# Optimization experiments

Hardware: AMD Instinct MI355X
Metric: run time of the kernel (lower is better)

Reference implementation:

```python
import jax, jax.numpy as jnp
import numpy as np

E = 512      # embed_dim
H = 8        # num_heads
D = E // H   # head_dim = 64
R = 32       # rot_dims (partial rotary)
THETA = 10000.0


def _rope(x):
    # x: [B, H, S, D]; rotate first R dims (interleaved pairs, lucidrains-style)
    S = x.shape[-2]
    inv_freq = THETA ** (-jnp.arange(0, R, 2, dtype=jnp.float32) / R)  # [R/2]
    ang = jnp.arange(S, dtype=jnp.float32)[:, None] * inv_freq          # [S, R/2]
    c, s = jnp.cos(ang), jnp.sin(ang)
    xr, xp = x[..., :R], x[..., R:]
    x1, x2 = xr[..., 0::2], xr[..., 1::2]
    rot = jnp.stack([x1 * c - x2 * s, x1 * s + x2 * c], axis=-1).reshape(xr.shape)
    return jnp.concatenate([rot, xp], axis=-1)


def setup_inputs() -> dict:
    key = jax.random.key(0)
    k1, k2, k3, k4 = jax.random.split(key, 4)
    B, S = 4, 2048
    x = jax.random.normal(k1, (B, S, E), dtype=jnp.float32)
    input_mask = jax.random.randint(k2, (B, S), 0, 2).astype(bool)
    W_in = jax.random.normal(k3, (3 * E, E), dtype=jnp.float32) / np.sqrt(E).astype(np.float32)
    W_out = jax.random.normal(k4, (E, E), dtype=jnp.float32) / np.sqrt(E).astype(np.float32)
    return {"x": x, "input_mask": input_mask, "W_in": W_in, "W_out": W_out}


def reference(x, input_mask, W_in, W_out):
    B, S, _ = x.shape
    # fused QKV projection (Linear, no bias): x @ W_in.T -> [B,S,3E]
    qkv = (x @ W_in.T).reshape(B, S, 3, H, D).transpose(2, 0, 3, 1, 4)  # [3,B,H,S,D]
    q, k, v = qkv[0], qkv[1], qkv[2]
    q = _rope(q)
    k = _rope(k)
    # mask: causal AND (both tokens valid OR diagonal)
    causal = jnp.tril(jnp.ones((S, S), dtype=bool))
    inv = ~input_mask                                  # [B,S]
    cross = inv[:, None, :] | inv[:, :, None]          # [B,S,S]
    square = (~cross) | jnp.eye(S, dtype=bool)         # diagonal forced True
    full = causal[None, :, :] & square                 # [B,S,S]
    scores = jnp.einsum('bhsd,bhtd->bhst', q, k) / np.float32(np.sqrt(D))
    scores = jnp.where(full[:, None, :, :], scores, -jnp.inf)
    probs = jax.nn.softmax(scores, axis=-1)
    attn = jnp.einsum('bhst,bhtd->bhsd', probs, v)
    attn = attn.transpose(0, 2, 1, 3).reshape(B, S, E)
    return attn @ W_out.T
```

## Files before the change

kernel.cpp:

```cpp
#include <hip/hip_runtime.h>
#include <math.h>

#define B_ 4
#define S_ 2048
#define E_ 512
#define H_ 8
#define D_ 64

typedef short bf16x8 __attribute__((ext_vector_type(8)));
typedef float f32x4 __attribute__((ext_vector_type(4)));

__device__ inline short f2bf(float f) {
  union { float f; unsigned u; } v; v.f = f;
  unsigned r = v.u + 0x7FFF + ((v.u >> 16) & 1);
  return (short)(r >> 16);
}
__device__ inline short f2bf_fast(float f) {
  union { float f; unsigned u; } v; v.f = f;
  return (short)((v.u + 0x8000u) >> 16);
}
__device__ inline float bf2f(short s) {
  union { unsigned u; float f; } v; v.u = ((unsigned)(unsigned short)s) << 16;
  return v.f;
}
__device__ __forceinline__ float exp2_hw(float x) {
  float r; asm("v_exp_f32 %0, %1" : "=v"(r) : "v"(x)); return r;
}

__device__ __forceinline__ void gload16(const short* g, short* l) {
  __builtin_amdgcn_global_load_lds(
      (__attribute__((address_space(1))) void*)g,
      (__attribute__((address_space(3))) void*)l, 16, 0, 0);
}

__global__ __launch_bounds__(256) void cvt_all(
    const float* __restrict__ x, const float* __restrict__ win,
    const float* __restrict__ wout, short* __restrict__ xb,
    short* __restrict__ winb, short* __restrict__ woutb) {
  int bid = blockIdx.x;
  const float* src; short* dst; int i;
  if (bid < 4096)      { src = x;    dst = xb;    i = bid * 256 + threadIdx.x; }
  else if (bid < 4864) { src = win;  dst = winb;  i = (bid - 4096) * 256 + threadIdx.x; }
  else                 { src = wout; dst = woutb; i = (bid - 4864) * 256 + threadIdx.x; }
  float4 f = ((const float4*)src)[i];
  short4 o;
  o.x = f2bf(f.x); o.y = f2bf(f.y); o.z = f2bf(f.z); o.w = f2bf(f.w);
  ((short4*)dst)[i] = o;
}

__global__ __launch_bounds__(256, 6) void gemm_qkv_mfma(
    const short* __restrict__ Xb,
    const short* __restrict__ Wb,
    short* __restrict__ qb, short* __restrict__ kb, short* __restrict__ vbT) {
  __shared__ __align__(16) short As[2 * 128 * 32];
  __shared__ __align__(16) short Bs[2 * 64 * 32];
  const int tid = threadIdx.x;
  const int w = tid >> 6, lane = tid & 63;
  const int l15 = lane & 15, quad = lane >> 4;
  const int wm = w & 1, wn = w >> 1;
  const int m0 = blockIdx.x * 128;
  const int n0 = blockIdx.y * 64;

  const int srow = tid >> 2, sch = (tid & 3) * 8;
  const short* gA0 = Xb + (size_t)(m0 + srow) * E_ + sch;
  const short* gA1 = Xb + (size_t)(m0 + srow + 64) * E_ + sch;
  const short* gB0 = Wb + (size_t)(n0 + srow) * E_ + sch;

  f32x4 acc[4][2];
  for (int mt = 0; mt < 4; ++mt)
    for (int nt = 0; nt < 2; ++nt) acc[mt][nt] = (f32x4){0.f, 0.f, 0.f, 0.f};

  gload16(gA0, &As[tid * 8]);
  gload16(gA1, &As[2048 + tid * 8]);
  gload16(gB0, &Bs[tid * 8]);
  gA0 += 32; gA1 += 32; gB0 += 32;
  __syncthreads();

  int cur = 0;
  for (int t = 0; t < 16; ++t) {
    if (t < 15) {
      const int nbA = (cur ^ 1) * 4096, nbB = (cur ^ 1) * 2048;
      gload16(gA0, &As[nbA + tid * 8]);
      gload16(gA1, &As[nbA + 2048 + tid * 8]);
      gload16(gB0, &Bs[nbB + tid * 8]);
      gA0 += 32; gA1 += 32; gB0 += 32;
    }
    const int cbA = cur * 4096, cbB = cur * 2048;
    bf16x8 a[4], bfr[2];
#pragma unroll
    for (int mt = 0; mt < 4; ++mt)
      a[mt] = *(const bf16x8*)&As[cbA + (wm * 64 + mt * 16 + l15) * 32 + quad * 8];
#pragma unroll
    for (int nt = 0; nt < 2; ++nt)
      bfr[nt] = *(const bf16x8*)&Bs[cbB + (wn * 32 + nt * 16 + l15) * 32 + quad * 8];
#pragma unroll
    for (int mt = 0; mt < 4; ++mt)
#pragma unroll
      for (int nt = 0; nt < 2; ++nt)
        acc[mt][nt] = __builtin_amdgcn_mfma_f32_16x16x32_bf16(a[mt], bfr[nt], acc[mt][nt], 0, 0, 0);
    __syncthreads();
    cur ^= 1;
  }

  const int t3 = n0 >> 9;
  for (int nt = 0; nt < 2; ++nt) {
    const int n = n0 + wn * 32 + nt * 16 + l15;
    const int h = (n >> 6) & 7;
    const int d = n & 63;
    const bool dorope = (t3 < 2) && (d < 32);
    const float sgn = (d & 1) ? 1.f : -1.f;
    const float fr = dorope ? exp2f((float)(d >> 1) * -0.8304820237f) : 0.f;
    for (int mt = 0; mt < 4; ++mt) {
      for (int i = 0; i < 4; ++i) {
        const int m = m0 + wm * 64 + mt * 16 + quad * 4 + i;
        const int b = m >> 11, s = m & (S_ - 1);
        float val = acc[mt][nt][i];
        float pv = __shfl_xor(val, 1, 64);
        float outv = val;
        if (dorope) {
          float ang = (float)s * fr;
          float sn, cs;
          sincosf(ang, &sn, &cs);
          outv = val * cs + pv * sgn * sn;
        }
        if (t3 == 2)
          vbT[((size_t)(b * 8 + h) * D_ + d) * S_ + s] = f2bf(outv);
        else {
          short* dst = (t3 == 0) ? qb : kb;
          dst[(((size_t)(b * 8 + h)) * S_ + s) * D_ + d] = f2bf(outv);
        }
      }
    }
  }
}

__global__ __launch_bounds__(256) void gemm_out_mfma(
    const short* __restrict__ Ab, const short* __restrict__ Wb,
    float* __restrict__ out) {
  __shared__ __align__(16) short As[2 * 128 * 32];
  __shared__ __align__(16) short Bs[2 * 64 * 32];
  const int tid = threadIdx.x;
  const int w = tid >> 6, lane = tid & 63;
  const int l15 = lane & 15, quad = lane >> 4;
  const int wm = w & 1, wn = w >> 1;
  const int m0 = blockIdx.x * 128;
  const int n0 = blockIdx.y * 64;

  const int srow = tid >> 2, sch = (tid & 3) * 8;
  const short* gA0 = Ab + (size_t)(m0 + srow) * E_ + sch;
  const short* gA1 = Ab + (size_t)(m0 + srow + 64) * E_ + sch;
  const short* gB0 = Wb + (size_t)(n0 + srow) * E_ + sch;

  f32x4 acc[4][2];
  for (int mt = 0; mt < 4; ++mt)
    for (int nt = 0; nt < 2; ++nt) acc[mt][nt] = (f32x4){0.f, 0.f, 0.f, 0.f};

  gload16(gA0, &As[tid * 8]);
  gload16(gA1, &As[2048 + tid * 8]);
  gload16(gB0, &Bs[tid * 8]);
  gA0 += 32; gA1 += 32; gB0 += 32;
  __syncthreads();

  int cur = 0;
  for (int t = 0; t < 16; ++t) {
    if (t < 15) {
      const int nbA = (cur ^ 1) * 4096, nbB = (cur ^ 1) * 2048;
      gload16(gA0, &As[nbA + tid * 8]);
      gload16(gA1, &As[nbA + 2048 + tid * 8]);
      gload16(gB0, &Bs[nbB + tid * 8]);
      gA0 += 32; gA1 += 32; gB0 += 32;
    }
    const int cbA = cur * 4096, cbB = cur * 2048;
    bf16x8 a[4], bfr[2];
#pragma unroll
    for (int mt = 0; mt < 4; ++mt)
      a[mt] = *(const bf16x8*)&As[cbA + (wm * 64 + mt * 16 + l15) * 32 + quad * 8];
#pragma unroll
    for (int nt = 0; nt < 2; ++nt)
      bfr[nt] = *(const bf16x8*)&Bs[cbB + (wn * 32 + nt * 16 + l15) * 32 + quad * 8];
#pragma unroll
    for (int mt = 0; mt < 4; ++mt)
#pragma unroll
      for (int nt = 0; nt < 2; ++nt)
        acc[mt][nt] = __builtin_amdgcn_mfma_f32_16x16x32_bf16(a[mt], bfr[nt], acc[mt][nt], 0, 0, 0);
    __syncthreads();
    cur ^= 1;
  }
  for (int mt = 0; mt < 4; ++mt)
    for (int nt = 0; nt < 2; ++nt) {
      const int n = n0 + wn * 32 + nt * 16 + l15;
      for (int i = 0; i < 4; ++i) {
        const int m = m0 + wm * 64 + mt * 16 + quad * 4 + i;
        out[(size_t)m * E_ + n] = acc[mt][nt][i];
      }
    }
}

__global__ __launch_bounds__(256) void flash_mfma(
    const short* __restrict__ qb, const short* __restrict__ kb,
    const short* __restrict__ vbT, const int* __restrict__ maskp,
    short* __restrict__ pb0, short* __restrict__ pb1,
    float* __restrict__ lb0, float* __restrict__ lb1,
    short* __restrict__ ob) {
  __shared__ __align__(16) short Ks[64][72];
  __shared__ __align__(16) short VT[64][72];
  __shared__ __align__(16) short Pl[4][16][72];
  __shared__ float kbias[64];
  const int tid = threadIdx.x;
  const int w = tid >> 6, lane = tid & 63;
  const int l15 = lane & 15, quad = lane >> 4;
  const int bid = blockIdx.x;
  const int u = bid & 7, v = bid >> 3;
  const int bh = (u << 2) | (v & 3);
  const int w2 = v >> 2;
  const int pair = w2 & 15;
  const int kh = w2 >> 4;
  const int b = bh >> 3, hd = bh & 7;
  const short* qbase = qb + (size_t)bh * S_ * D_;
  const short* kbase = kb + (size_t)bh * S_ * D_;
  const short* vtb   = vbT + (size_t)bh * D_ * S_;
  short* PB = kh ? pb1 : pb0;
  float* LB = kh ? lb1 : lb0;
  const float c2 = 0.1803368801f;
  bf16x8 ones;
  for (int j = 0; j < 8; ++j) ones[j] = (short)0x3F80;

  for (int seg = 0; seg < 2; ++seg) {
    const int qt = (seg == 0) ? pair : 31 - pair;
    const int r0 = qt * 64;
    const int mid = (qt + 2) >> 1;
    const int lo = kh ? mid : 0;
    const int hi = kh ? (qt + 1) : mid;
    bf16x8 aq[2];
    {
      const short* qrow = qbase + (size_t)(r0 + 16 * w + l15) * D_;
      aq[0] = *(const bf16x8*)&qrow[quad * 8];
      aq[1] = *(const bf16x8*)&qrow[32 + quad * 8];
    }
    f32x4 o[4], lsum;
    for (int no = 0; no < 4; ++no) o[no] = (f32x4){0.f, 0.f, 0.f, 0.f};
    lsum = (f32x4){0.f, 0.f, 0.f, 0.f};

    for (int kt = lo; kt < hi; ++kt) {
      const int t0 = kt * 64;
      __syncthreads();
      for (int l = 0; l < 2; ++l) {
        int idx = tid + 256 * l;
        int row = idx >> 3, ch = (idx & 7) * 8;
        *(bf16x8*)&Ks[row][ch] = *(const bf16x8*)(kbase + (size_t)(t0 + row) * D_ + ch);
        *(bf16x8*)&VT[row][ch] = *(const bf16x8*)(vtb + (size_t)row * S_ + t0 + ch);
      }
      if (tid < 64)
        kbias[tid] = maskp[b * S_ + t0 + tid] ? -23.08312f : -1.0e38f;
      __syncthreads();
      f32x4 sfr[4];
      for (int nb = 0; nb < 4; ++nb) sfr[nb] = (f32x4){0.f, 0.f, 0.f, 0.f};
      for (int nb = 0; nb < 4; ++nb)
        for (int ks = 0; ks < 2; ++ks) {
          bf16x8 bk = *(const bf16x8*)&Ks[l15 + 16 * nb][32 * ks + quad * 8];
          sfr[nb] = __builtin_amdgcn_mfma_f32_16x16x32_bf16(aq[ks], bk, sfr[nb], 0, 0, 0);
        }
      if (kt < qt) {
        for (int nb = 0; nb < 4; ++nb) {
          const float bb = kbias[l15 + 16 * nb];
          for (int i = 0; i < 4; ++i)
            Pl[w][quad * 4 + i][l15 + 16 * nb] = f2bf_fast(exp2_hw(sfr[nb][i] * c2 + bb));
        }
      } else {
        for (int nb = 0; nb < 4; ++nb) {
          const int tg = l15 + 16 * nb;
          const float bb = kbias[l15 + 16 * nb];
          for (int i = 0; i < 4; ++i) {
            const float bbi = (tg > 16 * w + quad * 4 + i) ? -1.0e38f : bb;
            Pl[w][quad * 4 + i][l15 + 16 * nb] = f2bf_fast(exp2_hw(sfr[nb][i] * c2 + bbi));
          }
        }
      }
      asm volatile("s_waitcnt lgkmcnt(0)" ::: "memory");
      bf16x8 ap0 = *(const bf16x8*)&Pl[w][l15][quad * 8];
      bf16x8 ap1 = *(const bf16x8*)&Pl[w][l15][32 + quad * 8];
      for (int no = 0; no < 4; ++no) {
        bf16x8 bv0 = *(const bf16x8*)&VT[16 * no + l15][quad * 8];
        bf16x8 bv1 = *(const bf16x8*)&VT[16 * no + l15][32 + quad * 8];
        o[no] = __builtin_amdgcn_mfma_f32_16x16x32_bf16(ap0, bv0, o[no], 0, 0, 0);
        o[no] = __builtin_amdgcn_mfma_f32_16x16x32_bf16(ap1, bv1, o[no], 0, 0, 0);
      }
      lsum = __builtin_amdgcn_mfma_f32_16x16x32_bf16(ap0, ones, lsum, 0, 0, 0);
      lsum = __builtin_amdgcn_mfma_f32_16x16x32_bf16(ap1, ones, lsum, 0, 0, 0);
    }
    for (int i = 0; i < 4; ++i) {
      const int s = r0 + 16 * w + quad * 4 + i;
      const int qm = maskp[b * S_ + s];
      const size_t row = (size_t)(b * S_ + s) * E_ + hd * D_;
      if (kh == 0 && !qm) {
        for (int no = 0; no < 4; ++no) {
          const int d = l15 + 16 * no;
          ob[row + d] = vtb[(size_t)d * S_ + s];
        }
      }
      for (int no = 0; no < 4; ++no)
        PB[row + l15 + 16 * no] = f2bf(o[no][i]);
      if (l15 == 0)
        LB[bh * S_ + s] = lsum[i];
    }
  }
}

__global__ __launch_bounds__(256) void merge_kernel(
    const short* __restrict__ pb0, const short* __restrict__ pb1,
    const float* __restrict__ lb0, const float* __restrict__ lb1,
    const int* __restrict__ maskp, short* __restrict__ ob) {
  int idx = blockIdx.x * 256 + threadIdx.x;
  int m = idx >> 6, e = (idx & 63) * 8;
  if (!maskp[m]) return;
  int b = m >> 11, s = m & (S_ - 1);
  int bh = b * 8 + (e >> 6);
  float l = lb0[bh * S_ + s] + lb1[bh * S_ + s];
  float inv = 1.f / l;
  bf16x8 p0 = *(const bf16x8*)&pb0[(size_t)m * E_ + e];
  bf16x8 p1 = *(const bf16x8*)&pb1[(size_t)m * E_ + e];
  bf16x8 r;
  for (int j = 0; j < 8; ++j)
    r[j] = f2bf((bf2f(p0[j]) + bf2f(p1[j])) * inv);
  *(bf16x8*)&ob[(size_t)m * E_ + e] = r;
}

extern "C" void kernel_launch(void* const* d_in, const int* in_sizes, int n_in,
                              void* d_out, int out_size, void* d_ws, size_t ws_size,
                              hipStream_t stream) {
  const float* x    = (const float*)d_in[0];
  const int*   mask = (const int*)d_in[1];
  const float* Win  = (const float*)d_in[2];
  const float* Wout = (const float*)d_in[3];
  float* out = (float*)d_out;

  short* Xb    = (short*)d_ws;
  short* Winb  = Xb + 8192 * 512;
  short* Woutb = Winb + 1536 * 512;
  short* qb    = Woutb + 512 * 512;
  short* kb    = qb + 32 * 2048 * 64;
  short* vbT   = kb + 32 * 2048 * 64;
  short* ob    = vbT + 32 * 2048 * 64;
  short* pb0   = ob + 8192 * 512;
  short* pb1   = pb0 + 8192 * 512;
  float* lb0   = (float*)(pb1 + 8192 * 512);
  float* lb1   = lb0 + 32 * 2048;

  cvt_all<<<5120, 256, 0, stream>>>(x, Win, Wout, Xb, Winb, Woutb);
  gemm_qkv_mfma<<<dim3(64, 24), 256, 0, stream>>>(Xb, Winb, qb, kb, vbT);
  flash_mfma<<<1024, 256, 0, stream>>>(qb, kb, vbT, mask, pb0, pb1, lb0, lb1, ob);
  merge_kernel<<<2048, 256, 0, stream>>>(pb0, pb1, lb0, lb1, mask, ob);
  gemm_out_mfma<<<dim3(64, 8), 256, 0, stream>>>(ob, Woutb, out);
}
```

Baseline: 162.1 us.

## Prefetch next K/V tile into registers and split flash grid per query tile

The flash kernel now loads the next K, V^T and mask tile into registers while the current tile's MFMAs run, then writes it to LDS after a barrier. This is meant to hide global-memory latency behind compute. Each block now handles one query tile instead of a paired low/high tile, which doubles the grid to 2048 blocks for more parallelism but drops the paired work balancing. LDS row padding also shrinks from 72 to 68 shorts. That changes bank mapping, but it leaves 16-byte vector LDS accesses only 8-byte aligned, which risks split or slower accesses.

```diff
diff --git a/kernel.cpp b/kernel.cpp
--- a/kernel.cpp
+++ b/kernel.cpp
@@ -202,9 +202,9 @@
     short* __restrict__ pb0, short* __restrict__ pb1,
     float* __restrict__ lb0, float* __restrict__ lb1,
     short* __restrict__ ob) {
-  __shared__ __align__(16) short Ks[64][72];
-  __shared__ __align__(16) short VT[64][72];
-  __shared__ __align__(16) short Pl[4][16][72];
+  __shared__ __align__(16) short Ks[64][68];
+  __shared__ __align__(16) short VT[64][68];
+  __shared__ __align__(16) short Pl[4][16][68];
   __shared__ float kbias[64];
   const int tid = threadIdx.x;
   const int w = tid >> 6, lane = tid & 63;
@@ -213,8 +213,8 @@
   const int u = bid & 7, v = bid >> 3;
   const int bh = (u << 2) | (v & 3);
   const int w2 = v >> 2;
-  const int pair = w2 & 15;
-  const int kh = w2 >> 4;
+  const int qt = w2 & 31;
+  const int kh = w2 >> 5;
   const int b = bh >> 3, hd = bh & 7;
   const short* qbase = qb + (size_t)bh * S_ * D_;
   const short* kbase = kb + (size_t)bh * S_ * D_;
@@ -225,34 +225,50 @@
   bf16x8 ones;
   for (int j = 0; j < 8; ++j) ones[j] = (short)0x3F80;
 
-  for (int seg = 0; seg < 2; ++seg) {
-    const int qt = (seg == 0) ? pair : 31 - pair;
-    const int r0 = qt * 64;
-    const int mid = (qt + 2) >> 1;
-    const int lo = kh ? mid : 0;
-    const int hi = kh ? (qt + 1) : mid;
-    bf16x8 aq[2];
+  const int r0 = qt * 64;
+  const int mid = (qt + 2) >> 1;
+  const int lo = kh ? mid : 0;
+  const int hi = kh ? (qt + 1) : mid;
+
+  bf16x8 aq[2];
+  {
+    const short* qrow = qbase + (size_t)(r0 + 16 * w + l15) * D_;
+    aq[0] = *(const bf16x8*)&qrow[quad * 8];
+    aq[1] = *(const bf16x8*)&qrow[32 + quad * 8];
+  }
+  f32x4 o[4], lsum;
+  for (int no = 0; no < 4; ++no) o[no] = (f32x4){0.f, 0.f, 0.f, 0.f};
+  lsum = (f32x4){0.f, 0.f, 0.f, 0.f};
+
+  const int srow = tid >> 3, sch = (tid & 7) * 8;
+
+  if (lo < hi) {
+    bf16x8 sk0, sk1, sv0, sv1; int mv = 0;
     {
-      const short* qrow = qbase + (size_t)(r0 + 16 * w + l15) * D_;
-      aq[0] = *(const bf16x8*)&qrow[quad * 8];
-      aq[1] = *(const bf16x8*)&qrow[32 + quad * 8];
-    }
-    f32x4 o[4], lsum;
-    for (int no = 0; no < 4; ++no) o[no] = (f32x4){0.f, 0.f, 0.f, 0.f};
-    lsum = (f32x4){0.f, 0.f, 0.f, 0.f};
+      const int t0 = lo * 64;
+      sk0 = *(const bf16x8*)(kbase + (size_t)(t0 + srow) * D_ + sch);
+      sk1 = *(const bf16x8*)(kbase + (size_t)(t0 + srow + 32) * D_ + sch);
+      sv0 = *(const bf16x8*)(vtb + (size_t)srow * S_ + t0 + sch);
+      sv1 = *(const bf16x8*)(vtb + (size_t)(srow + 32) * S_ + t0 + sch);
+      if (tid < 64) mv = maskp[b * S_ + t0 + tid];
+    }
+    *(bf16x8*)&Ks[srow][sch]      = sk0;
+    *(bf16x8*)&Ks[srow + 32][sch] = sk1;
+    *(bf16x8*)&VT[srow][sch]      = sv0;
+    *(bf16x8*)&VT[srow + 32][sch] = sv1;
+    if (tid < 64) kbias[tid] = mv ? -23.08312f : -1.0e38f;
+    __syncthreads();
 
     for (int kt = lo; kt < hi; ++kt) {
-      const int t0 = kt * 64;
-      __syncthreads();
-      for (int l = 0; l < 2; ++l) {
-        int idx = tid + 256 * l;
-        int row = idx >> 3, ch = (idx & 7) * 8;
-        *(bf16x8*)&Ks[row][ch] = *(const bf16x8*)(kbase + (size_t)(t0 + row) * D_ + ch);
-        *(bf16x8*)&VT[row][ch] = *(const bf16x8*)(vtb + (size_t)row * S_ + t0 + ch);
-      }
-      if (tid < 64)
-        kbias[tid] = maskp[b * S_ + t0 + tid] ? -23.08312f : -1.0e38f;
-      __syncthreads();
+      const bool pre = (kt + 1 < hi);
+      if (pre) {
+        const int t1 = (kt + 1) * 64;
+        sk0 = *(const bf16x8*)(kbase + (size_t)(t1 + srow) * D_ + sch);
+        sk1 = *(const bf16x8*)(kbase + (size_t)(t1 + srow + 32) * D_ + sch);
+        sv0 = *(const bf16x8*)(vtb + (size_t)srow * S_ + t1 + sch);
+        sv1 = *(const bf16x8*)(vtb + (size_t)(srow + 32) * S_ + t1 + sch);
+        if (tid < 64) mv = maskp[b * S_ + t1 + tid];
+      }
       f32x4 sfr[4];
       for (int nb = 0; nb < 4; ++nb) sfr[nb] = (f32x4){0.f, 0.f, 0.f, 0.f};
       for (int nb = 0; nb < 4; ++nb)
@@ -287,22 +303,32 @@
       }
       lsum = __builtin_amdgcn_mfma_f32_16x16x32_bf16(ap0, ones, lsum, 0, 0, 0);
       lsum = __builtin_amdgcn_mfma_f32_16x16x32_bf16(ap1, ones, lsum, 0, 0, 0);
-    }
-    for (int i = 0; i < 4; ++i) {
-      const int s = r0 + 16 * w + quad * 4 + i;
-      const int qm = maskp[b * S_ + s];
-      const size_t row = (size_t)(b * S_ + s) * E_ + hd * D_;
-      if (kh == 0 && !qm) {
-        for (int no = 0; no < 4; ++no) {
-          const int d = l15 + 16 * no;
-          ob[row + d] = vtb[(size_t)d * S_ + s];
-        }
-      }
-      for (int no = 0; no < 4; ++no)
-        PB[row + l15 + 16 * no] = f2bf(o[no][i]);
-      if (l15 == 0)
-        LB[bh * S_ + s] = lsum[i];
-    }
+      __syncthreads();
+      if (pre) {
+        *(bf16x8*)&Ks[srow][sch]      = sk0;
+        *(bf16x8*)&Ks[srow + 32][sch] = sk1;
+        *(bf16x8*)&VT[srow][sch]      = sv0;
+        *(bf16x8*)&VT[srow + 32][sch] = sv1;
+        if (tid < 64) kbias[tid] = mv ? -23.08312f : -1.0e38f;
+      }
+      __syncthreads();
+    }
+  }
+
+  for (int i = 0; i < 4; ++i) {
+    const int s = r0 + 16 * w + quad * 4 + i;
+    const int qm = maskp[b * S_ + s];
+    const size_t row = (size_t)(b * S_ + s) * E_ + hd * D_;
+    if (kh == 0 && !qm) {
+      for (int no = 0; no < 4; ++no) {
+        const int d = l15 + 16 * no;
+        ob[row + d] = vtb[(size_t)d * S_ + s];
+      }
+    }
+    for (int no = 0; no < 4; ++no)
+      PB[row + l15 + 16 * no] = f2bf(o[no][i]);
+    if (l15 == 0)
+      LB[bh * S_ + s] = lsum[i];
   }
 }
 
@@ -348,7 +374,7 @@
 
   cvt_all<<<5120, 256, 0, stream>>>(x, Win, Wout, Xb, Winb, Woutb);
   gemm_qkv_mfma<<<dim3(64, 24), 256, 0, stream>>>(Xb, Winb, qb, kb, vbT);
-  flash_mfma<<<1024, 256, 0, stream>>>(qb, kb, vbT, mask, pb0, pb1, lb0, lb1, ob);
+  flash_mfma<<<2048, 256, 0, stream>>>(qb, kb, vbT, mask, pb0, pb1, lb0, lb1, ob);
   merge_kernel<<<2048, 256, 0, stream>>>(pb0, pb1, lb0, lb1, mask, ob);
   gemm_out_mfma<<<dim3(64, 8), 256, 0, stream>>>(ob, Woutb, out);
 }
```

Result: slower. 169.1 us (+4.4%).
